# Kernel tuning notes

Hardware: AMD Instinct MI355X
Metric: run time of the kernel (lower is better)

## Reference

```python
import jax, jax.numpy as jnp
import numpy as np
from jax import lax

SEQ_LEN, BC, NODES, FEAT, HID, NUM_LAYER = 12, 16, 1024, 32, 64, 2
NEG_BIG = -1e16


def _gru_layer(x_seq, w_ih, w_hh, b_ih, b_hh):
    # x_seq: [T, B, in]; PyTorch gate order r, z, n
    B = x_seq.shape[1]
    h0 = jnp.zeros((B, w_hh.shape[1]), dtype=x_seq.dtype)

    def step(h, x):
        gi = x @ w_ih.T + b_ih
        gh = h @ w_hh.T + b_hh
        ir, iz, inn = jnp.split(gi, 3, axis=-1)
        hr, hz, hn = jnp.split(gh, 3, axis=-1)
        r = jax.nn.sigmoid(ir + hr)
        zg = jax.nn.sigmoid(iz + hz)
        n = jnp.tanh(inn + r * hn)
        h_new = (1.0 - zg) * n + zg * h
        return h_new, h_new

    h_T, ys = lax.scan(step, h0, x_seq)
    return ys, h_T


def _gat_aggregate(z_, maskf):
    # z_: [bc, nodes, H]; inner-product attention with leaky_relu(0.1) and adjacency mask
    att = jnp.einsum('bnd,bmd->bnm', z_, z_)
    att = jax.nn.leaky_relu(att, negative_slope=0.1) * maskf[None]
    att = jnp.where(att == 0.0, NEG_BIG, att)  # masked_fill_(atten==0, -1e16)
    att = jax.nn.softmax(att, axis=2)
    return jnp.einsum('bnm,bmd->bnd', att, z_)


def setup_inputs() -> dict:
    key = jax.random.key(0)
    ks = jax.random.split(key, 12)
    s = 1.0 / np.sqrt(HID)
    inp = {
        'h': jax.random.normal(ks[0], (SEQ_LEN, BC, NODES, FEAT), dtype=jnp.float32),
        'mask': jax.random.randint(ks[1], (NODES, NODES), 0, 2, dtype=jnp.int32),
        'w_ih0': jax.random.uniform(ks[2], (3 * HID, FEAT), minval=-s, maxval=s),
        'w_hh0': jax.random.uniform(ks[3], (3 * HID, HID), minval=-s, maxval=s),
        'b_ih0': jax.random.uniform(ks[4], (3 * HID,), minval=-s, maxval=s),
        'b_hh0': jax.random.uniform(ks[5], (3 * HID,), minval=-s, maxval=s),
        'w_ih1': jax.random.uniform(ks[6], (3 * HID, HID), minval=-s, maxval=s),
        'w_hh1': jax.random.uniform(ks[7], (3 * HID, HID), minval=-s, maxval=s),
        'b_ih1': jax.random.uniform(ks[8], (3 * HID,), minval=-s, maxval=s),
        'b_hh1': jax.random.uniform(ks[9], (3 * HID,), minval=-s, maxval=s),
    }
    return inp


def reference(h, mask, w_ih0, w_hh0, b_ih0, b_hh0, w_ih1, w_hh1, b_ih1, b_hh1):
    x = h.reshape(SEQ_LEN, BC * NODES, FEAT)
    ys0, hT0 = _gru_layer(x, w_ih0, w_hh0, b_ih0, b_hh0)
    _, hT1 = _gru_layer(ys0, w_ih1, w_hh1, b_ih1, b_hh1)
    # z: [num_layer, bc, nodes, H]
    z = jnp.stack([hT0, hT1]).reshape(NUM_LAYER, BC, NODES, HID)
    maskf = mask.astype(z.dtype)
    h_agg = jax.vmap(_gat_aggregate, in_axes=(0, None))(z, maskf)
    return h_agg  # [num_layer, bc, nodes, H]
```

## Files before the change

kernel.cpp:

```cpp
#include <hip/hip_runtime.h>
#include <math.h>

#define SEQ 12
#define NBATCH 16384
#define FEAT 32
#define HID 64
#define NSPLIT 4

#define WP_IH0 0
#define WP_HH0 6144
#define WP_IH1 18432
#define WP_HH1 30720
#define WP_TOTAL 43008

typedef __attribute__((ext_vector_type(8))) short bf16x8;
typedef __attribute__((ext_vector_type(4))) float f32x4;

#define MFMA_B16(A,B,C) __builtin_amdgcn_mfma_f32_16x16x32_bf16((A),(B),(C),0,0,0)

union B8u { unsigned short s[8]; bf16x8 v; };

__device__ __forceinline__ float sigf(float x) { return 1.0f / (1.0f + __expf(-x)); }
__device__ __forceinline__ float tanh_fast(float x) { return 2.0f / (1.0f + __expf(-2.0f * x)) - 1.0f; }

__device__ __forceinline__ unsigned int packsplit(float v) {
  unsigned int u  = __float_as_uint(v);
  unsigned int hi = u & 0xFFFF0000u;
  unsigned int lo = __float_as_uint(v - __uint_as_float(hi)) >> 16;
  return hi | lo;
}

__device__ __forceinline__ void unpack8(const unsigned int* p, bf16x8& H, bf16x8& L) {
  uint4 u0 = *(const uint4*)p;
  uint4 u1 = *(const uint4*)(p + 4);
  unsigned int uu[8] = {u0.x, u0.y, u0.z, u0.w, u1.x, u1.y, u1.z, u1.w};
  B8u hh, ll;
  #pragma unroll
  for (int i = 0; i < 8; i++) {
    hh.s[i] = (unsigned short)(uu[i] >> 16);
    ll.s[i] = (unsigned short)(uu[i] & 0xFFFFu);
  }
  H = hh.v; L = ll.v;
}

__device__ __forceinline__ void split8(const float* fa, bf16x8& H, bf16x8& L) {
  B8u hh, ll;
  #pragma unroll
  for (int i = 0; i < 8; i++) {
    unsigned int u  = __float_as_uint(fa[i]);
    unsigned int hi = u & 0xFFFF0000u;
    hh.s[i] = (unsigned short)(hi >> 16);
    ll.s[i] = (unsigned short)(__float_as_uint(fa[i] - __uint_as_float(hi)) >> 16);
  }
  H = hh.v; L = ll.v;
}

#define DOT4(acc, A_, B_)                                   \
  acc = fmaf((A_).x, (B_).x, acc);                          \
  acc = fmaf((A_).y, (B_).y, acc);                          \
  acc = fmaf((A_).z, (B_).z, acc);                          \
  acc = fmaf((A_).w, (B_).w, acc);

__global__ void prep_frag_kernel(const float* __restrict__ w_ih0, const float* __restrict__ w_hh0,
                                 const float* __restrict__ w_ih1, const float* __restrict__ w_hh1,
                                 unsigned short* __restrict__ wf)
{
  int i = blockIdx.x * blockDim.x + threadIdx.x;
  if (i >= 43008) return;
  const float* src; int K, rel, baseS;
  if (i < 6144)       { src = w_ih0; K = 32; rel = i;         baseS = 0; }
  else if (i < 18432) { src = w_hh0; K = 64; rel = i - 6144;  baseS = 12288; }
  else if (i < 30720) { src = w_ih1; K = 64; rel = i - 18432; baseS = 36864; }
  else                { src = w_hh1; K = 64; rel = i - 30720; baseS = 61440; }
  int nks = K / 32;
  int fp   = rel >> 9;
  int lane = (rel >> 3) & 63;
  int e    = rel & 7;
  int ct = fp / nks, ks = fp % nks;
  int g = ct * 16 + (lane & 15);
  int k = ks * 32 + (lane >> 4) * 8 + e;
  float v = src[g * K + k];
  unsigned int u = __float_as_uint(v);
  unsigned short hi = (unsigned short)(u >> 16);
  float hif = __uint_as_float(u & 0xFFFF0000u);
  unsigned short lo = (unsigned short)(__float_as_uint(v - hif) >> 16);
  int out = baseS + fp * 1024 + lane * 8 + e;
  wf[out]       = hi;
  wf[out + 512] = lo;
}

__global__ __launch_bounds__(256, 2) void gru_fused(
    const float* __restrict__ x, const unsigned short* __restrict__ wf,
    const float* __restrict__ b_ih0, const float* __restrict__ b_hh0,
    const float* __restrict__ b_ih1, const float* __restrict__ b_hh1,
    unsigned int* __restrict__ zpk0, unsigned int* __restrict__ zpk1)
{
  __shared__ unsigned int h0l[2][16 * 68];
  __shared__ unsigned int h1l[2][16 * 68];
  const int tid = threadIdx.x;
  const int w = tid >> 6, l = tid & 63, lr = l & 15, lg = l >> 4;
  const int s0 = blockIdx.x * 16;
  const int j = w * 16 + lr;

  bf16x8 Wih0[3][2], Whh0[3][2][2], Wih1[3][2][2], Whh1[3][2][2];
  #pragma unroll
  for (int g = 0; g < 3; g++) {
    const int ct = w + g * 4;
    Wih0[g][0] = *(const bf16x8*)&wf[ct * 1024 + l * 8];
    Wih0[g][1] = *(const bf16x8*)&wf[ct * 1024 + 512 + l * 8];
    #pragma unroll
    for (int ks = 0; ks < 2; ks++) {
      Whh0[g][ks][0] = *(const bf16x8*)&wf[12288 + (ct * 2 + ks) * 1024 + l * 8];
      Whh0[g][ks][1] = *(const bf16x8*)&wf[12288 + (ct * 2 + ks) * 1024 + 512 + l * 8];
      Wih1[g][ks][0] = *(const bf16x8*)&wf[36864 + (ct * 2 + ks) * 1024 + l * 8];
      Wih1[g][ks][1] = *(const bf16x8*)&wf[36864 + (ct * 2 + ks) * 1024 + 512 + l * 8];
      Whh1[g][ks][0] = *(const bf16x8*)&wf[61440 + (ct * 2 + ks) * 1024 + l * 8];
      Whh1[g][ks][1] = *(const bf16x8*)&wf[61440 + (ct * 2 + ks) * 1024 + 512 + l * 8];
    }
  }

  const float br0  = b_ih0[j]      + b_hh0[j];
  const float bz0  = b_ih0[64 + j] + b_hh0[64 + j];
  const float bni0 = b_ih0[128 + j];
  const float bnh0 = b_hh0[128 + j];
  const float br1  = b_ih1[j]      + b_hh1[j];
  const float bz1  = b_ih1[64 + j] + b_hh1[64 + j];
  const float bni1 = b_ih1[128 + j];
  const float bnh1 = b_hh1[128 + j];

  for (int i = tid; i < 1088; i += 256) { h0l[0][i] = 0u; h1l[0][i] = 0u; }
  float hD0[4] = {0.f, 0.f, 0.f, 0.f};
  float hD1[4] = {0.f, 0.f, 0.f, 0.f};
  __syncthreads();

  float4 xc0 = *(const float4*)(x + ((size_t)s0 + lr) * FEAT + lg * 8);
  float4 xc1 = *(const float4*)(x + ((size_t)s0 + lr) * FEAT + lg * 8 + 4);

  int pb = 0;
  #pragma unroll 1
  for (int t = 0; t < SEQ; t++) {
    const int cb = pb ^ 1;
    float4 xn0, xn1;
    if (t < SEQ - 1) {
      const float* xp = x + ((size_t)(t + 1) * NBATCH + s0 + lr) * FEAT + lg * 8;
      xn0 = *(const float4*)xp;
      xn1 = *(const float4*)(xp + 4);
    }

    f32x4 aR, aZ, aNI, aNH;
    #pragma unroll
    for (int e = 0; e < 4; e++) { aR[e] = br0; aZ[e] = bz0; aNI[e] = bni0; aNH[e] = bnh0; }
    {
      float fa[8] = {xc0.x, xc0.y, xc0.z, xc0.w, xc1.x, xc1.y, xc1.z, xc1.w};
      bf16x8 Ah, Al;
      split8(fa, Ah, Al);
      aR  = MFMA_B16(Ah, Wih0[0][0], aR);  aR  = MFMA_B16(Al, Wih0[0][0], aR);  aR  = MFMA_B16(Ah, Wih0[0][1], aR);
      aZ  = MFMA_B16(Ah, Wih0[1][0], aZ);  aZ  = MFMA_B16(Al, Wih0[1][0], aZ);  aZ  = MFMA_B16(Ah, Wih0[1][1], aZ);
      aNI = MFMA_B16(Ah, Wih0[2][0], aNI); aNI = MFMA_B16(Al, Wih0[2][0], aNI); aNI = MFMA_B16(Ah, Wih0[2][1], aNI);
    }
    #pragma unroll
    for (int ks = 0; ks < 2; ks++) {
      bf16x8 Ah, Al;
      unpack8(&h0l[pb][lr * 68 + ks * 32 + lg * 8], Ah, Al);
      aR  = MFMA_B16(Ah, Whh0[0][ks][0], aR);  aR  = MFMA_B16(Al, Whh0[0][ks][0], aR);  aR  = MFMA_B16(Ah, Whh0[0][ks][1], aR);
      aZ  = MFMA_B16(Ah, Whh0[1][ks][0], aZ);  aZ  = MFMA_B16(Al, Whh0[1][ks][0], aZ);  aZ  = MFMA_B16(Ah, Whh0[1][ks][1], aZ);
      aNH = MFMA_B16(Ah, Whh0[2][ks][0], aNH); aNH = MFMA_B16(Al, Whh0[2][ks][0], aNH); aNH = MFMA_B16(Ah, Whh0[2][ks][1], aNH);
    }
    #pragma unroll
    for (int e = 0; e < 4; e++) {
      float rg = sigf(aR[e]);
      float zg = sigf(aZ[e]);
      float n  = tanh_fast(fmaf(rg, aNH[e], aNI[e]));
      float hn = fmaf(zg, hD0[e] - n, n);
      hD0[e] = hn;
      h0l[cb][(lg * 4 + e) * 68 + j] = packsplit(hn);
    }
    __syncthreads();

    #pragma unroll
    for (int e = 0; e < 4; e++) { aR[e] = br1; aZ[e] = bz1; aNI[e] = bni1; aNH[e] = bnh1; }
    #pragma unroll
    for (int ks = 0; ks < 2; ks++) {
      bf16x8 Ah, Al;
      unpack8(&h0l[cb][lr * 68 + ks * 32 + lg * 8], Ah, Al);
      aR  = MFMA_B16(Ah, Wih1[0][ks][0], aR);  aR  = MFMA_B16(Al, Wih1[0][ks][0], aR);  aR  = MFMA_B16(Ah, Wih1[0][ks][1], aR);
      aZ  = MFMA_B16(Ah, Wih1[1][ks][0], aZ);  aZ  = MFMA_B16(Al, Wih1[1][ks][0], aZ);  aZ  = MFMA_B16(Ah, Wih1[1][ks][1], aZ);
      aNI = MFMA_B16(Ah, Wih1[2][ks][0], aNI); aNI = MFMA_B16(Al, Wih1[2][ks][0], aNI); aNI = MFMA_B16(Ah, Wih1[2][ks][1], aNI);
    }
    #pragma unroll
    for (int ks = 0; ks < 2; ks++) {
      bf16x8 Ah, Al;
      unpack8(&h1l[pb][lr * 68 + ks * 32 + lg * 8], Ah, Al);
      aR  = MFMA_B16(Ah, Whh1[0][ks][0], aR);  aR  = MFMA_B16(Al, Whh1[0][ks][0], aR);  aR  = MFMA_B16(Ah, Whh1[0][ks][1], aR);
      aZ  = MFMA_B16(Ah, Whh1[1][ks][0], aZ);  aZ  = MFMA_B16(Al, Whh1[1][ks][0], aZ);  aZ  = MFMA_B16(Ah, Whh1[1][ks][1], aZ);
      aNH = MFMA_B16(Ah, Whh1[2][ks][0], aNH); aNH = MFMA_B16(Al, Whh1[2][ks][0], aNH); aNH = MFMA_B16(Ah, Whh1[2][ks][1], aNH);
    }
    #pragma unroll
    for (int e = 0; e < 4; e++) {
      float rg = sigf(aR[e]);
      float zg = sigf(aZ[e]);
      float n  = tanh_fast(fmaf(rg, aNH[e], aNI[e]));
      float hn = fmaf(zg, hD1[e] - n, n);
      hD1[e] = hn;
      h1l[cb][(lg * 4 + e) * 68 + j] = packsplit(hn);
    }
    if (t == SEQ - 1) {
      #pragma unroll
      for (int e = 0; e < 4; e++) {
        int sl = lg * 4 + e;
        zpk0[(size_t)(s0 + sl) * 64 + j] = packsplit(hD0[e]);
        zpk1[(size_t)(s0 + sl) * 64 + j] = packsplit(hD1[e]);
      }
    }
    __syncthreads();
    xc0 = xn0; xc1 = xn1;
    pb = cb;
  }
}

__global__ void prep_kernel(const float* __restrict__ w_ih0, const float* __restrict__ w_hh0,
                            const float* __restrict__ w_ih1, const float* __restrict__ w_hh1,
                            float* __restrict__ wp)
{
  for (int i = blockIdx.x * blockDim.x + threadIdx.x; i < WP_TOTAL; i += gridDim.x * blockDim.x) {
    const float* src;
    int K, rel;
    if (i < WP_HH0)      { src = w_ih0; K = 32; rel = i; }
    else if (i < WP_IH1) { src = w_hh0; K = 64; rel = i - WP_HH0; }
    else if (i < WP_HH1) { src = w_ih1; K = 64; rel = i - WP_IH1; }
    else                 { src = w_hh1; K = 64; rel = i - WP_HH1; }
    int kr = rel & 3;
    int jj = (rel >> 2) & 63;
    int rest = rel >> 8;
    int g = rest % 3;
    int k4 = rest / 3;
    wp[i] = src[(g * 64 + jj) * K + k4 * 4 + kr];
  }
}

__global__ __launch_bounds__(256, 1) void gru_fallback(
    const float* __restrict__ x, const float* __restrict__ wpack,
    const float* __restrict__ b_ih0, const float* __restrict__ b_hh0,
    const float* __restrict__ b_ih1, const float* __restrict__ b_hh1,
    unsigned int* __restrict__ zout)
{
  __shared__ float wlds[36864];
  __shared__ float h0s[16][64];
  __shared__ float h1s[16][64];
  const int tid = threadIdx.x;
  {
    const float4* src = (const float4*)(wpack + WP_HH0);
    float4* dst = (float4*)wlds;
    #pragma unroll 4
    for (int i = tid; i < 9216; i += 256) dst[i] = src[i];
  }
  const int j  = tid & 63;
  const int sg = __builtin_amdgcn_readfirstlane(tid >> 6);
  const float br0  = b_ih0[j]      + b_hh0[j];
  const float bz0  = b_ih0[64 + j] + b_hh0[64 + j];
  const float bni0 = b_ih0[128 + j];
  const float bnh0 = b_hh0[128 + j];
  const float br1  = b_ih1[j]      + b_hh1[j];
  const float bz1  = b_ih1[64 + j] + b_hh1[64 + j];
  const float bni1 = b_ih1[128 + j];
  const float bnh1 = b_hh1[128 + j];
  const int s0 = blockIdx.x * 16;
  float h0r[4] = {0.f, 0.f, 0.f, 0.f};
  float h1r[4] = {0.f, 0.f, 0.f, 0.f};
  #pragma unroll
  for (int ss = 0; ss < 4; ss++) { h0s[sg * 4 + ss][j] = 0.f; h1s[sg * 4 + ss][j] = 0.f; }
  __syncthreads();
  const float4* wih0g = (const float4*)(wpack + WP_IH0);
  const float4* whh0l = (const float4*)(wlds);
  const float4* wih1l = (const float4*)(wlds + 12288);
  const float4* whh1l = (const float4*)(wlds + 24576);
  for (int t = 0; t < SEQ; t++) {
    float ar[4], az[4], ani[4], anh[4];
    #pragma unroll
    for (int ss = 0; ss < 4; ss++) { ar[ss] = br0; az[ss] = bz0; ani[ss] = bni0; anh[ss] = bnh0; }
    const float4* xr0 = (const float4*)(x + ((size_t)t * NBATCH + (s0 + sg * 4 + 0)) * FEAT);
    const float4* xr1 = (const float4*)(x + ((size_t)t * NBATCH + (s0 + sg * 4 + 1)) * FEAT);
    const float4* xr2 = (const float4*)(x + ((size_t)t * NBATCH + (s0 + sg * 4 + 2)) * FEAT);
    const float4* xr3 = (const float4*)(x + ((size_t)t * NBATCH + (s0 + sg * 4 + 3)) * FEAT);
    #pragma unroll
    for (int k4 = 0; k4 < 8; k4++) {
      float4 wr = wih0g[(k4 * 3 + 0) * 64 + j];
      float4 wz = wih0g[(k4 * 3 + 1) * 64 + j];
      float4 wn = wih0g[(k4 * 3 + 2) * 64 + j];
      float4 xv[4] = {xr0[k4], xr1[k4], xr2[k4], xr3[k4]};
      #pragma unroll
      for (int ss = 0; ss < 4; ss++) {
        DOT4(ar[ss],  wr, xv[ss]);
        DOT4(az[ss],  wz, xv[ss]);
        DOT4(ani[ss], wn, xv[ss]);
      }
    }
    #pragma unroll
    for (int k4 = 0; k4 < 16; k4++) {
      float4 wr = whh0l[(k4 * 3 + 0) * 64 + j];
      float4 wz = whh0l[(k4 * 3 + 1) * 64 + j];
      float4 wn = whh0l[(k4 * 3 + 2) * 64 + j];
      #pragma unroll
      for (int ss = 0; ss < 4; ss++) {
        float4 hv = *(const float4*)&h0s[sg * 4 + ss][k4 * 4];
        DOT4(ar[ss],  wr, hv);
        DOT4(az[ss],  wz, hv);
        DOT4(anh[ss], wn, hv);
      }
    }
    float h0n[4];
    #pragma unroll
    for (int ss = 0; ss < 4; ss++) {
      float rg = sigf(ar[ss]);
      float zg = sigf(az[ss]);
      float ng = tanh_fast(fmaf(rg, anh[ss], ani[ss]));
      h0n[ss] = fmaf(zg, h0r[ss] - ng, ng);
    }
    __syncthreads();
    #pragma unroll
    for (int ss = 0; ss < 4; ss++) { h0s[sg * 4 + ss][j] = h0n[ss]; h0r[ss] = h0n[ss]; }
    __syncthreads();
    #pragma unroll
    for (int ss = 0; ss < 4; ss++) { ar[ss] = br1; az[ss] = bz1; ani[ss] = bni1; anh[ss] = bnh1; }
    #pragma unroll
    for (int k4 = 0; k4 < 16; k4++) {
      float4 wr = wih1l[(k4 * 3 + 0) * 64 + j];
      float4 wz = wih1l[(k4 * 3 + 1) * 64 + j];
      float4 wn = wih1l[(k4 * 3 + 2) * 64 + j];
      #pragma unroll
      for (int ss = 0; ss < 4; ss++) {
        float4 hv = *(const float4*)&h0s[sg * 4 + ss][k4 * 4];
        DOT4(ar[ss],  wr, hv);
        DOT4(az[ss],  wz, hv);
        DOT4(ani[ss], wn, hv);
      }
    }
    #pragma unroll
    for (int k4 = 0; k4 < 16; k4++) {
      float4 wr = whh1l[(k4 * 3 + 0) * 64 + j];
      float4 wz = whh1l[(k4 * 3 + 1) * 64 + j];
      float4 wn = whh1l[(k4 * 3 + 2) * 64 + j];
      #pragma unroll
      for (int ss = 0; ss < 4; ss++) {
        float4 hv = *(const float4*)&h1s[sg * 4 + ss][k4 * 4];
        DOT4(ar[ss],  wr, hv);
        DOT4(az[ss],  wz, hv);
        DOT4(anh[ss], wn, hv);
      }
    }
    float h1n[4];
    #pragma unroll
    for (int ss = 0; ss < 4; ss++) {
      float rg = sigf(ar[ss]);
      float zg = sigf(az[ss]);
      float ng = tanh_fast(fmaf(rg, anh[ss], ani[ss]));
      h1n[ss] = fmaf(zg, h1r[ss] - ng, ng);
    }
    __syncthreads();
    #pragma unroll
    for (int ss = 0; ss < 4; ss++) { h1s[sg * 4 + ss][j] = h1n[ss]; h1r[ss] = h1n[ss]; }
    __syncthreads();
  }
  #pragma unroll
  for (int ss = 0; ss < 4; ss++) {
    int s = s0 + sg * 4 + ss;
    zout[(size_t)s * 64 + j]            = packsplit(h0r[ss]);
    zout[(size_t)(NBATCH + s) * 64 + j] = packsplit(h1r[ss]);
  }
}

__global__ __launch_bounds__(256, 4) void gat_mfma3(
    const unsigned int* __restrict__ zpk, const int* __restrict__ mask,
    float* __restrict__ partO, float* __restrict__ partMD,
    float* __restrict__ out, int nsplit)
{
  __shared__ unsigned int VT[64 * 68];
  __shared__ float        PS[64 * 68];
  const int tid = threadIdx.x;
  const int w = tid >> 6, l = tid & 63, lr = l & 15, lg = l >> 4;
  const int blk  = blockIdx.x;
  const int lbrt = blk / nsplit;
  const int half = blk - lbrt * nsplit;
  const int rt = lbrt & 15;
  const int lb = lbrt >> 4;
  const int tiles = 16 / nsplit;
  const int mt0 = half * tiles;
  const unsigned int* zb = zpk + (size_t)lb * 65536;
  const int n0 = rt * 64;

  bf16x8 Qh[2], Ql[2];
  #pragma unroll
  for (int ks = 0; ks < 2; ks++)
    unpack8(&zb[(size_t)(n0 + w * 16 + lr) * 64 + ks * 32 + lg * 8], Qh[ks], Ql[ks]);

  f32x4 O[4];
  float M[4], D[4];
  #pragma unroll
  for (int ct = 0; ct < 4; ct++)
    #pragma unroll
    for (int e = 0; e < 4; e++) O[ct][e] = 0.f;
  #pragma unroll
  for (int e = 0; e < 4; e++) { M[e] = -INFINITY; D[e] = 0.f; }

  #pragma unroll 1
  for (int mt = mt0; mt < mt0 + tiles; ++mt) {
    __syncthreads();
    {
      unsigned int tmp[16];
      #pragma unroll
      for (int r = 0; r < 16; r++)
        tmp[r] = zb[(size_t)(mt * 64 + w * 16 + r) * 64 + l];
      #pragma unroll
      for (int q = 0; q < 4; q++)
        *(uint4*)&VT[l * 68 + w * 16 + q * 4] =
            make_uint4(tmp[q * 4], tmp[q * 4 + 1], tmp[q * 4 + 2], tmp[q * 4 + 3]);
    }
    __syncthreads();

    f32x4 S[4];
    #pragma unroll
    for (int ct = 0; ct < 4; ct++)
      #pragma unroll
      for (int e = 0; e < 4; e++) S[ct][e] = 0.f;
    #pragma unroll
    for (int ks = 0; ks < 2; ks++) {
      #pragma unroll
      for (int ct = 0; ct < 4; ct++) {
        bf16x8 Kh, Kl;
        unpack8(&zb[(size_t)(mt * 64 + ct * 16 + lr) * 64 + ks * 32 + lg * 8], Kh, Kl);
        S[ct] = MFMA_B16(Qh[ks], Kh, S[ct]);
        S[ct] = MFMA_B16(Ql[ks], Kh, S[ct]);
        S[ct] = MFMA_B16(Qh[ks], Kl, S[ct]);
      }
    }

    #pragma unroll
    for (int ct = 0; ct < 4; ct++) {
      #pragma unroll
      for (int e = 0; e < 4; e++) {
        int mm = mask[(size_t)(n0 + w * 16 + lg * 4 + e) * 1024 + mt * 64 + ct * 16 + lr];
        float v = S[ct][e];
        float lrv = v > 0.f ? v : 0.1f * v;
        float a = mm ? lrv : 0.f;
        S[ct][e] = (a == 0.f) ? -1e16f : a;
      }
    }

    #pragma unroll
    for (int e = 0; e < 4; e++) {
      float m = fmaxf(fmaxf(S[0][e], S[1][e]), fmaxf(S[2][e], S[3][e]));
      #pragma unroll
      for (int sw = 1; sw < 16; sw <<= 1) m = fmaxf(m, __shfl_xor(m, sw, 16));
      float newM = fmaxf(M[e], m);
      float sc = __expf(M[e] - newM);
      float ps = 0.f;
      float pv[4];
      #pragma unroll
      for (int ct = 0; ct < 4; ct++) {
        pv[ct] = __expf(S[ct][e] - newM);
        ps += pv[ct];
      }
      #pragma unroll
      for (int sw = 1; sw < 16; sw <<= 1) ps += __shfl_xor(ps, sw, 16);
      D[e] = D[e] * sc + ps;
      M[e] = newM;
      #pragma unroll
      for (int ct = 0; ct < 4; ct++) {
        O[ct][e] *= sc;
        PS[(w * 16 + lg * 4 + e) * 68 + ct * 16 + lr] = pv[ct];
      }
    }

    #pragma unroll
    for (int ks = 0; ks < 2; ks++) {
      const float* pp = &PS[(w * 16 + lr) * 68 + ks * 32 + lg * 8];
      float4 p0 = *(const float4*)pp;
      float4 p1 = *(const float4*)(pp + 4);
      float fa[8] = {p0.x, p0.y, p0.z, p0.w, p1.x, p1.y, p1.z, p1.w};
      bf16x8 Ph, Pl;
      split8(fa, Ph, Pl);
      #pragma unroll
      for (int ct = 0; ct < 4; ct++) {
        bf16x8 Vh, Vl;
        unpack8(&VT[(ct * 16 + lr) * 68 + ks * 32 + lg * 8], Vh, Vl);
        O[ct] = MFMA_B16(Ph, Vh, O[ct]);
        O[ct] = MFMA_B16(Pl, Vh, O[ct]);
        O[ct] = MFMA_B16(Ph, Vl, O[ct]);
      }
    }
  }

  if (nsplit == 1) {
    #pragma unroll
    for (int e = 0; e < 4; e++) {
      float inv = 1.0f / D[e];
      size_t rowo = ((size_t)lb * 1024 + n0 + w * 16 + lg * 4 + e) * 64;
      #pragma unroll
      for (int ct = 0; ct < 4; ct++)
        out[rowo + ct * 16 + lr] = O[ct][e] * inv;
    }
  } else {
    float* po = partO + (size_t)blk * 4096;
    #pragma unroll
    for (int e = 0; e < 4; e++) {
      int row = w * 16 + lg * 4 + e;
      #pragma unroll
      for (int ct = 0; ct < 4; ct++)
        po[row * 64 + ct * 16 + lr] = O[ct][e];
      if (lr == 0) {
        partMD[(size_t)blk * 128 + row]      = M[e];
        partMD[(size_t)blk * 128 + 64 + row] = D[e];
      }
    }
  }
}

__global__ __launch_bounds__(256) void gat_combine(
    const float* __restrict__ partO, const float* __restrict__ partMD,
    float* __restrict__ out, int nsplit)
{
  const int lbrt = blockIdx.x;
  const int q  = threadIdx.x >> 2;
  const int dc = (threadIdx.x & 3) * 16;
  float Ms[NSPLIT], Ds[NSPLIT];
  float M = -INFINITY;
  for (int i = 0; i < nsplit; i++) {
    Ms[i] = partMD[(size_t)(lbrt * nsplit + i) * 128 + q];
    Ds[i] = partMD[(size_t)(lbrt * nsplit + i) * 128 + 64 + q];
    M = fmaxf(M, Ms[i]);
  }
  float s[NSPLIT], dt = 0.f;
  for (int i = 0; i < nsplit; i++) { s[i] = __expf(Ms[i] - M); dt = fmaf(Ds[i], s[i], dt); }
  float inv = 1.0f / dt;
  float* op = out + ((size_t)lbrt * 64 + q) * 64 + dc;
  #pragma unroll
  for (int v = 0; v < 4; v++) {
    float4 acc = make_float4(0.f, 0.f, 0.f, 0.f);
    for (int i = 0; i < nsplit; i++) {
      const float4 o = *(const float4*)(partO + (size_t)(lbrt * nsplit + i) * 4096 + q * 64 + dc + v * 4);
      acc.x = fmaf(o.x, s[i], acc.x); acc.y = fmaf(o.y, s[i], acc.y);
      acc.z = fmaf(o.z, s[i], acc.z); acc.w = fmaf(o.w, s[i], acc.w);
    }
    *(float4*)(op + v * 4) = make_float4(acc.x * inv, acc.y * inv, acc.z * inv, acc.w * inv);
  }
}

extern "C" void kernel_launch(void* const* d_in, const int* in_sizes, int n_in,
                              void* d_out, int out_size, void* d_ws, size_t ws_size,
                              hipStream_t stream) {
  const float* h     = (const float*)d_in[0];
  const int*   mask  = (const int*)d_in[1];
  const float* w_ih0 = (const float*)d_in[2];
  const float* w_hh0 = (const float*)d_in[3];
  const float* b_ih0 = (const float*)d_in[4];
  const float* b_hh0 = (const float*)d_in[5];
  const float* w_ih1 = (const float*)d_in[6];
  const float* w_hh1 = (const float*)d_in[7];
  const float* b_ih1 = (const float*)d_in[8];
  const float* b_hh1 = (const float*)d_in[9];
  float* out = (float*)d_out;

  char* wsb = (char*)d_ws;
  unsigned int* zpk = (unsigned int*)wsb;
  const size_t Z_BYTES  = (size_t)2 * NBATCH * 64 * 4;
  const size_t PART_OFF = Z_BYTES + 176128;
  const size_t NEED_FAST = PART_OFF
      + (size_t)512 * NSPLIT * 4096 * 4
      + (size_t)512 * NSPLIT * 128 * 4;

  if (ws_size >= NEED_FAST) {
    unsigned short* wfrag = (unsigned short*)(wsb + Z_BYTES);
    float* partO  = (float*)(wsb + PART_OFF);
    float* partMD = (float*)(wsb + PART_OFF + (size_t)512 * NSPLIT * 4096 * 4);
    prep_frag_kernel<<<168, 256, 0, stream>>>(w_ih0, w_hh0, w_ih1, w_hh1, wfrag);
    gru_fused<<<1024, 256, 0, stream>>>(h, wfrag, b_ih0, b_hh0, b_ih1, b_hh1,
                                        zpk, zpk + (size_t)NBATCH * 64);
    gat_mfma3<<<512 * NSPLIT, 256, 0, stream>>>(zpk, mask, partO, partMD, out, NSPLIT);
    gat_combine<<<512, 256, 0, stream>>>(partO, partMD, out, NSPLIT);
  } else {
    float* wpack = (float*)(wsb + Z_BYTES);
    prep_kernel<<<24, 256, 0, stream>>>(w_ih0, w_hh0, w_ih1, w_hh1, wpack);
    gru_fallback<<<1024, 256, 0, stream>>>(h, wpack, b_ih0, b_hh0, b_ih1, b_hh1, zpk);
    gat_mfma3<<<512, 256, 0, stream>>>(zpk, mask, nullptr, nullptr, out, 1);
  }
}
```

Before: 197.9 us.

## Bitpack mask, use fixed softmax shift, drop P low-part MFMA in GAT

Packs the int32 adjacency mask into bits in a small pre-kernel so the attention kernel reads 2 words per row instead of 16 ints per tile row. Replaces the online-softmax running max and rescaling with a constant shift of 64, valid because GRU hidden states are bounded by 1 in 64 dims. This also simplifies the split combine to plain sums. P is rounded to a single bf16 and its low-part MFMA is removed, trading accuracy for fewer MFMAs; fully masked rows would now give division by zero.

```diff
diff --git a/kernel.cpp b/kernel.cpp
--- a/kernel.cpp
+++ b/kernel.cpp
@@ -89,6 +89,18 @@
   wf[out + 512] = lo;
 }
 
+__global__ void mask_pack(const int* __restrict__ mask, unsigned int* __restrict__ mbits)
+{
+  int i = blockIdx.x * blockDim.x + threadIdx.x;
+  if (i >= 32768) return;
+  int r = i >> 5, wd = i & 31;
+  const int* mp = mask + (size_t)r * 1024 + wd * 32;
+  unsigned int b = 0;
+  #pragma unroll
+  for (int k = 0; k < 32; k++) b |= (mp[k] != 0 ? 1u : 0u) << k;
+  mbits[i] = b;
+}
+
 __global__ __launch_bounds__(256, 2) void gru_fused(
     const float* __restrict__ x, const unsigned short* __restrict__ wf,
     const float* __restrict__ b_ih0, const float* __restrict__ b_hh0,
@@ -369,9 +381,9 @@
   }
 }
 
-__global__ __launch_bounds__(256, 4) void gat_mfma3(
-    const unsigned int* __restrict__ zpk, const int* __restrict__ mask,
-    float* __restrict__ partO, float* __restrict__ partMD,
+__global__ __launch_bounds__(256, 4) void gat_mfma4(
+    const unsigned int* __restrict__ zpk, const unsigned int* __restrict__ mbits,
+    float* __restrict__ partO, float* __restrict__ partD,
     float* __restrict__ out, int nsplit)
 {
   __shared__ unsigned int VT[64 * 68];
@@ -394,13 +406,11 @@
     unpack8(&zb[(size_t)(n0 + w * 16 + lr) * 64 + ks * 32 + lg * 8], Qh[ks], Ql[ks]);
 
   f32x4 O[4];
-  float M[4], D[4];
+  float D[4] = {0.f, 0.f, 0.f, 0.f};
   #pragma unroll
   for (int ct = 0; ct < 4; ct++)
     #pragma unroll
     for (int e = 0; e < 4; e++) O[ct][e] = 0.f;
-  #pragma unroll
-  for (int e = 0; e < 4; e++) { M[e] = -INFINITY; D[e] = 0.f; }
 
   #pragma unroll 1
   for (int mt = mt0; mt < mt0 + tiles; ++mt) {
@@ -435,40 +445,20 @@
     }
 
     #pragma unroll
-    for (int ct = 0; ct < 4; ct++) {
-      #pragma unroll
-      for (int e = 0; e < 4; e++) {
-        int mm = mask[(size_t)(n0 + w * 16 + lg * 4 + e) * 1024 + mt * 64 + ct * 16 + lr];
+    for (int e = 0; e < 4; e++) {
+      const int row = n0 + w * 16 + lg * 4 + e;
+      const uint2 mw = *(const uint2*)&mbits[(size_t)row * 32 + mt * 2];
+      const unsigned int sel[4] = {mw.x >> lr, mw.x >> (16 + lr), mw.y >> lr, mw.y >> (16 + lr)};
+      float ds = 0.f;
+      #pragma unroll
+      for (int ct = 0; ct < 4; ct++) {
         float v = S[ct][e];
         float lrv = v > 0.f ? v : 0.1f * v;
-        float a = mm ? lrv : 0.f;
-        S[ct][e] = (a == 0.f) ? -1e16f : a;
-      }
-    }
-
-    #pragma unroll
-    for (int e = 0; e < 4; e++) {
-      float m = fmaxf(fmaxf(S[0][e], S[1][e]), fmaxf(S[2][e], S[3][e]));
-      #pragma unroll
-      for (int sw = 1; sw < 16; sw <<= 1) m = fmaxf(m, __shfl_xor(m, sw, 16));
-      float newM = fmaxf(M[e], m);
-      float sc = __expf(M[e] - newM);
-      float ps = 0.f;
-      float pv[4];
-      #pragma unroll
-      for (int ct = 0; ct < 4; ct++) {
-        pv[ct] = __expf(S[ct][e] - newM);
-        ps += pv[ct];
-      }
-      #pragma unroll
-      for (int sw = 1; sw < 16; sw <<= 1) ps += __shfl_xor(ps, sw, 16);
-      D[e] = D[e] * sc + ps;
-      M[e] = newM;
-      #pragma unroll
-      for (int ct = 0; ct < 4; ct++) {
-        O[ct][e] *= sc;
-        PS[(w * 16 + lg * 4 + e) * 68 + ct * 16 + lr] = pv[ct];
-      }
+        float p = ((sel[ct] & 1u) && lrv != 0.0f) ? __expf(lrv - 64.0f) : 0.0f;
+        ds += p;
+        PS[(w * 16 + lg * 4 + e) * 68 + ct * 16 + lr] = p;
+      }
+      D[e] += ds;
     }
 
     #pragma unroll
@@ -477,17 +467,25 @@
       float4 p0 = *(const float4*)pp;
       float4 p1 = *(const float4*)(pp + 4);
       float fa[8] = {p0.x, p0.y, p0.z, p0.w, p1.x, p1.y, p1.z, p1.w};
-      bf16x8 Ph, Pl;
-      split8(fa, Ph, Pl);
+      B8u H;
+      #pragma unroll
+      for (int i = 0; i < 8; i++)
+        H.s[i] = (unsigned short)((__float_as_uint(fa[i]) + 0x8000u) >> 16);
+      bf16x8 Ph = H.v;
       #pragma unroll
       for (int ct = 0; ct < 4; ct++) {
         bf16x8 Vh, Vl;
         unpack8(&VT[(ct * 16 + lr) * 68 + ks * 32 + lg * 8], Vh, Vl);
         O[ct] = MFMA_B16(Ph, Vh, O[ct]);
-        O[ct] = MFMA_B16(Pl, Vh, O[ct]);
         O[ct] = MFMA_B16(Ph, Vl, O[ct]);
       }
     }
+  }
+
+  #pragma unroll
+  for (int e = 0; e < 4; e++) {
+    #pragma unroll
+    for (int sw = 1; sw < 16; sw <<= 1) D[e] += __shfl_xor(D[e], sw, 16);
   }
 
   if (nsplit == 1) {
@@ -507,30 +505,20 @@
       #pragma unroll
       for (int ct = 0; ct < 4; ct++)
         po[row * 64 + ct * 16 + lr] = O[ct][e];
-      if (lr == 0) {
-        partMD[(size_t)blk * 128 + row]      = M[e];
-        partMD[(size_t)blk * 128 + 64 + row] = D[e];
-      }
+      if (lr == 0) partD[(size_t)blk * 64 + row] = D[e];
     }
   }
 }
 
 __global__ __launch_bounds__(256) void gat_combine(
-    const float* __restrict__ partO, const float* __restrict__ partMD,
+    const float* __restrict__ partO, const float* __restrict__ partD,
     float* __restrict__ out, int nsplit)
 {
   const int lbrt = blockIdx.x;
   const int q  = threadIdx.x >> 2;
   const int dc = (threadIdx.x & 3) * 16;
-  float Ms[NSPLIT], Ds[NSPLIT];
-  float M = -INFINITY;
-  for (int i = 0; i < nsplit; i++) {
-    Ms[i] = partMD[(size_t)(lbrt * nsplit + i) * 128 + q];
-    Ds[i] = partMD[(size_t)(lbrt * nsplit + i) * 128 + 64 + q];
-    M = fmaxf(M, Ms[i]);
-  }
-  float s[NSPLIT], dt = 0.f;
-  for (int i = 0; i < nsplit; i++) { s[i] = __expf(Ms[i] - M); dt = fmaf(Ds[i], s[i], dt); }
+  float dt = 0.f;
+  for (int i = 0; i < nsplit; i++) dt += partD[(size_t)(lbrt * nsplit + i) * 64 + q];
   float inv = 1.0f / dt;
   float* op = out + ((size_t)lbrt * 64 + q) * 64 + dc;
   #pragma unroll
@@ -538,8 +526,7 @@
     float4 acc = make_float4(0.f, 0.f, 0.f, 0.f);
     for (int i = 0; i < nsplit; i++) {
       const float4 o = *(const float4*)(partO + (size_t)(lbrt * nsplit + i) * 4096 + q * 64 + dc + v * 4);
-      acc.x = fmaf(o.x, s[i], acc.x); acc.y = fmaf(o.y, s[i], acc.y);
-      acc.z = fmaf(o.z, s[i], acc.z); acc.w = fmaf(o.w, s[i], acc.w);
+      acc.x += o.x; acc.y += o.y; acc.z += o.z; acc.w += o.w;
     }
     *(float4*)(op + v * 4) = make_float4(acc.x * inv, acc.y * inv, acc.z * inv, acc.w * inv);
   }
@@ -564,23 +551,28 @@
   unsigned int* zpk = (unsigned int*)wsb;
   const size_t Z_BYTES  = (size_t)2 * NBATCH * 64 * 4;
   const size_t PART_OFF = Z_BYTES + 176128;
-  const size_t NEED_FAST = PART_OFF
-      + (size_t)512 * NSPLIT * 4096 * 4
-      + (size_t)512 * NSPLIT * 128 * 4;
+  const size_t PO_BYTES = (size_t)512 * NSPLIT * 4096 * 4;
+  const size_t PD_BYTES = (size_t)512 * NSPLIT * 64 * 4;
+  const size_t MB_OFF   = PART_OFF + PO_BYTES + PD_BYTES;
+  const size_t NEED_FAST = MB_OFF + 131072;
 
   if (ws_size >= NEED_FAST) {
     unsigned short* wfrag = (unsigned short*)(wsb + Z_BYTES);
     float* partO  = (float*)(wsb + PART_OFF);
-    float* partMD = (float*)(wsb + PART_OFF + (size_t)512 * NSPLIT * 4096 * 4);
+    float* partD  = (float*)(wsb + PART_OFF + PO_BYTES);
+    unsigned int* mbits = (unsigned int*)(wsb + MB_OFF);
     prep_frag_kernel<<<168, 256, 0, stream>>>(w_ih0, w_hh0, w_ih1, w_hh1, wfrag);
+    mask_pack<<<128, 256, 0, stream>>>(mask, mbits);
     gru_fused<<<1024, 256, 0, stream>>>(h, wfrag, b_ih0, b_hh0, b_ih1, b_hh1,
                                         zpk, zpk + (size_t)NBATCH * 64);
-    gat_mfma3<<<512 * NSPLIT, 256, 0, stream>>>(zpk, mask, partO, partMD, out, NSPLIT);
-    gat_combine<<<512, 256, 0, stream>>>(partO, partMD, out, NSPLIT);
+    gat_mfma4<<<512 * NSPLIT, 256, 0, stream>>>(zpk, mbits, partO, partD, out, NSPLIT);
+    gat_combine<<<512, 256, 0, stream>>>(partO, partD, out, NSPLIT);
   } else {
     float* wpack = (float*)(wsb + Z_BYTES);
+    unsigned int* mbits = (unsigned int*)(wsb + Z_BYTES + 172032);
     prep_kernel<<<24, 256, 0, stream>>>(w_ih0, w_hh0, w_ih1, w_hh1, wpack);
+    mask_pack<<<128, 256, 0, stream>>>(mask, mbits);
     gru_fallback<<<1024, 256, 0, stream>>>(h, wpack, b_ih0, b_hh0, b_ih1, b_hh1, zpk);
-    gat_mfma3<<<512, 256, 0, stream>>>(zpk, mask, nullptr, nullptr, out, 1);
-  }
-}
+    gat_mfma4<<<512, 256, 0, stream>>>(zpk, mbits, nullptr, nullptr, out, 1);
+  }
+}
```

After: 180.5 us. -8.8%, faster.
